# Kernel optimization log

Measured on AMD Instinct MI355X. Metric: run time of the kernel, lower is better.

The kernel has to match this reference:

```python
import jax, jax.numpy as jnp
import numpy as np

DIM = 768
INNER = int(DIM * 0.125)  # 96
N_TOK = 8
EPS = 1e-5


def setup_inputs() -> dict:
    key = jax.random.key(0)
    ks = jax.random.split(key, 5)
    x = jax.random.normal(ks[0], (64, DIM, 32, 32), dtype=jnp.float32)
    gamma = jnp.ones((DIM,), jnp.float32)
    beta = jnp.zeros((DIM,), jnp.float32)
    w1 = jax.random.normal(ks[1], (DIM, INNER), jnp.float32) * 0.02
    b1 = jnp.zeros((INNER,), jnp.float32)
    w2 = jax.random.normal(ks[2], (INNER, N_TOK), jnp.float32) * 0.02
    b2 = jnp.zeros((N_TOK,), jnp.float32)
    return {"x": x, "gamma": gamma, "beta": beta, "w1": w1, "b1": b1, "w2": w2, "b2": b2}


def reference(x, gamma, beta, w1, b1, w2, b2):
    B, C, H, W = x.shape
    # torch: x.transpose(1, 3).reshape(B, H*W, C)  ([B,C,H,W] -> [B,W,H,C] -> [B,HW,C])
    t = jnp.transpose(x, (0, 3, 2, 1)).reshape(B, H * W, C)
    # LayerNorm over channel dim
    mu = jnp.mean(t, axis=-1, keepdims=True)
    var = jnp.mean(jnp.square(t - mu), axis=-1, keepdims=True)
    xn = (t - mu) * jax.lax.rsqrt(var + EPS) * gamma + beta  # [B, HW, C]
    # small MLP producing per-token attention logits
    h = jax.nn.gelu(xn @ w1 + b1, approximate=False)  # [B, HW, INNER]
    attn = jax.nn.softmax(h @ w2 + b2, axis=1)        # softmax across HW -> [B, HW, N]
    # (x.unsqueeze(-1) * attn).mean(dim=1) == einsum / HW, no [B,HW,C,N] intermediate
    out = jnp.einsum('bhc,bhn->bcn', xn, attn) / (H * W)  # [B, C, N]
    return out
```

## Files before the change

kernel.cpp:

```cpp
#include <hip/hip_runtime.h>
#include <math.h>

#define BATCH 64
#define CH    768
#define NP    1024
#define NI    96
#define NT    8
#define EPSF  1e-5f

typedef __attribute__((ext_vector_type(8))) short  short8;
typedef __attribute__((ext_vector_type(4))) float  f32x4;

__device__ __forceinline__ unsigned short f2bf(float f) {
    unsigned int u = __float_as_uint(f);
    u += 0x7FFFu + ((u >> 16) & 1u);
    return (unsigned short)(u >> 16);
}

__global__ __launch_bounds__(64) void k_w1pack(const float* __restrict__ w1,
                                               unsigned short* __restrict__ w1f) {
    int ks = blockIdx.x / 6, nt = blockIdx.x % 6;
    int l  = threadIdx.x;
    int n  = nt * 16 + (l & 15);
    int k0 = ks * 32 + (l >> 4) * 8;
    unsigned short o[8];
#pragma unroll
    for (int j = 0; j < 8; ++j) o[j] = f2bf(w1[(size_t)(k0 + j) * NI + n]);
    unsigned short* dst = w1f + ((size_t)blockIdx.x * 64 + l) * 8;
#pragma unroll
    for (int j = 0; j < 8; ++j) dst[j] = o[j];
}

__global__ __launch_bounds__(256) void k_stats(const float* __restrict__ x,
                                               float2* __restrict__ stats) {
    int bid = blockIdx.x;
    int b   = bid >> 4;
    int p0  = (bid & 15) << 6;
    int lt  = threadIdx.x & 15;
    int cg  = threadIdx.x >> 4;
    const float* xb = x + (size_t)b * CH * NP + p0 + lt * 4;
    float4 s = make_float4(0.f,0.f,0.f,0.f);
    float4 q = make_float4(0.f,0.f,0.f,0.f);
#pragma unroll 4
    for (int c = cg; c < CH; c += 16) {
        float4 v = *(const float4*)(xb + (size_t)c * NP);
        s.x += v.x; s.y += v.y; s.z += v.z; s.w += v.w;
        q.x += v.x*v.x; q.y += v.y*v.y; q.z += v.z*v.z; q.w += v.w*v.w;
    }
    __shared__ float4 ls[16][16];
    __shared__ float4 lq[16][16];
    ls[cg][lt] = s; lq[cg][lt] = q;
    __syncthreads();
    for (int st = 8; st > 0; st >>= 1) {
        if (cg < st) {
            float4 s2 = ls[cg + st][lt], q2 = lq[cg + st][lt];
            s.x += s2.x; s.y += s2.y; s.z += s2.z; s.w += s2.w;
            q.x += q2.x; q.y += q2.y; q.z += q2.z; q.w += q2.w;
            ls[cg][lt] = s; lq[cg][lt] = q;
        }
        __syncthreads();
    }
    if (cg == 0) {
        const float inv = 1.0f / (float)CH;
        float2* st = stats + (size_t)b * NP + p0 + lt * 4;
        float mu, var;
        mu = s.x * inv; var = q.x * inv - mu * mu; st[0] = make_float2(mu, rsqrtf(var + EPSF));
        mu = s.y * inv; var = q.y * inv - mu * mu; st[1] = make_float2(mu, rsqrtf(var + EPSF));
        mu = s.z * inv; var = q.z * inv - mu * mu; st[2] = make_float2(mu, rsqrtf(var + EPSF));
        mu = s.w * inv; var = q.w * inv - mu * mu; st[3] = make_float2(mu, rsqrtf(var + EPSF));
    }
}

__global__ __launch_bounds__(256) void k_mlp(const float* __restrict__ x,
        const float2* __restrict__ stats,
        const float* __restrict__ gamma, const float* __restrict__ beta,
        const unsigned short* __restrict__ w1f,
        const float* __restrict__ b1, const float* __restrict__ w2,
        const float* __restrict__ b2, float* __restrict__ logits)
{
    int bid  = blockIdx.x;
    int b    = bid >> 3;
    int p0   = (bid & 7) << 7;
    int wv   = threadIdx.x >> 6;
    int lane = threadIdx.x & 63;
    int m    = lane & 15;
    int kg   = lane >> 4;
    int mt   = p0 + wv * 32;

    float2 st0 = stats[(size_t)b * NP + mt + m];
    float2 st1 = stats[(size_t)b * NP + mt + 16 + m];
    const float* xb = x + (size_t)b * CH * NP + mt + m;

    f32x4 accA[6], accB[6];
#pragma unroll
    for (int nt = 0; nt < 6; ++nt) {
        accA[nt] = (f32x4){0.f,0.f,0.f,0.f};
        accB[nt] = (f32x4){0.f,0.f,0.f,0.f};
    }
    const short8* wfp = (const short8*)w1f;

    for (int ks = 0; ks < 24; ++ks) {
        int cb = ks * 32 + kg * 8;
        const float* xc = xb + (size_t)cb * NP;
        float xv0[8], xv1[8];
#pragma unroll
        for (int j = 0; j < 8; ++j) {
            xv0[j] = xc[(size_t)j * NP];
            xv1[j] = xc[(size_t)j * NP + 16];
        }
        float4 g0 = *(const float4*)(gamma + cb);
        float4 g1 = *(const float4*)(gamma + cb + 4);
        float4 e0 = *(const float4*)(beta  + cb);
        float4 e1 = *(const float4*)(beta  + cb + 4);
        float gm[8] = {g0.x,g0.y,g0.z,g0.w,g1.x,g1.y,g1.z,g1.w};
        float bt[8] = {e0.x,e0.y,e0.z,e0.w,e1.x,e1.y,e1.z,e1.w};
        short8 a0, a1;
#pragma unroll
        for (int j = 0; j < 8; ++j) {
            float r0 = st0.y * gm[j];
            float r1 = st1.y * gm[j];
            float x0 = fmaf(xv0[j], r0, bt[j] - st0.x * r0);
            float x1 = fmaf(xv1[j], r1, bt[j] - st1.x * r1);
            a0[j] = (short)f2bf(x0);
            a1[j] = (short)f2bf(x1);
        }
        const short8* wk = wfp + (size_t)ks * 6 * 64 + lane;
#pragma unroll
        for (int nt = 0; nt < 6; ++nt) {
            short8 bf = wk[nt * 64];
            accA[nt] = __builtin_amdgcn_mfma_f32_16x16x32_bf16(a0, bf, accA[nt], 0, 0, 0);
            accB[nt] = __builtin_amdgcn_mfma_f32_16x16x32_bf16(a1, bf, accB[nt], 0, 0, 0);
        }
    }

    int nlo = lane & 15;
    float4 b2a = *(const float4*)b2;
    float4 b2b = *(const float4*)(b2 + 4);
#pragma unroll
    for (int half = 0; half < 2; ++half) {
        float lg[4][8];
#pragma unroll
        for (int r = 0; r < 4; ++r)
#pragma unroll
            for (int t = 0; t < 8; ++t) lg[r][t] = 0.f;
#pragma unroll
        for (int nt = 0; nt < 6; ++nt) {
            int n = nt * 16 + nlo;
            float b1v = b1[n];
            float4 w2a = *(const float4*)(w2 + n * 8);
            float4 w2b = *(const float4*)(w2 + n * 8 + 4);
            f32x4 ac = half ? accB[nt] : accA[nt];
#pragma unroll
            for (int r = 0; r < 4; ++r) {
                float h = ac[r] + b1v;
                h = 0.5f * h * (1.0f + erff(h * 0.70710678118654752f));
                lg[r][0] += h * w2a.x; lg[r][1] += h * w2a.y;
                lg[r][2] += h * w2a.z; lg[r][3] += h * w2a.w;
                lg[r][4] += h * w2b.x; lg[r][5] += h * w2b.y;
                lg[r][6] += h * w2b.z; lg[r][7] += h * w2b.w;
            }
        }
#pragma unroll
        for (int mask = 1; mask <= 8; mask <<= 1)
#pragma unroll
            for (int r = 0; r < 4; ++r)
#pragma unroll
                for (int t = 0; t < 8; ++t)
                    lg[r][t] += __shfl_xor(lg[r][t], mask, 64);
        if (nlo == 0) {
#pragma unroll
            for (int r = 0; r < 4; ++r) {
                int pp = mt + half * 16 + kg * 4 + r;
                float* op = logits + ((size_t)b * NP + pp) * NT;
                *(float4*)op       = make_float4(lg[r][0] + b2a.x, lg[r][1] + b2a.y,
                                                 lg[r][2] + b2a.z, lg[r][3] + b2a.w);
                *(float4*)(op + 4) = make_float4(lg[r][4] + b2b.x, lg[r][5] + b2b.y,
                                                 lg[r][6] + b2b.z, lg[r][7] + b2b.w);
            }
        }
    }
}

__global__ __launch_bounds__(256) void k_out(const float* __restrict__ x,
        const float* __restrict__ logits, const float2* __restrict__ stats,
        const float* __restrict__ gamma, const float* __restrict__ beta,
        float* __restrict__ out)
{
    int b   = blockIdx.x / 12;
    int c0  = (blockIdx.x % 12) * 64;
    int tid = threadIdx.x;
    int lane = tid & 63, wv = tid >> 6;
    __shared__ float gT[NT][NP];
    __shared__ float red[4][16];

    const float* lgp = logits + (size_t)b * NP * NT;
    const float2* stb = stats + (size_t)b * NP;
    float e[4][NT];
    float2 st4[4];
#pragma unroll
    for (int k = 0; k < 4; ++k) {
        int p = tid + 256 * k;
        float4 a  = *(const float4*)(lgp + (size_t)p * NT);
        float4 bq = *(const float4*)(lgp + (size_t)p * NT + 4);
        e[k][0]=a.x; e[k][1]=a.y; e[k][2]=a.z; e[k][3]=a.w;
        e[k][4]=bq.x; e[k][5]=bq.y; e[k][6]=bq.z; e[k][7]=bq.w;
        st4[k] = stb[p];
    }
    float mx[NT];
#pragma unroll
    for (int t = 0; t < NT; ++t)
        mx[t] = fmaxf(fmaxf(e[0][t], e[1][t]), fmaxf(e[2][t], e[3][t]));
#pragma unroll
    for (int mask = 1; mask <= 32; mask <<= 1)
#pragma unroll
        for (int t = 0; t < NT; ++t)
            mx[t] = fmaxf(mx[t], __shfl_xor(mx[t], mask, 64));
    if (lane == 0) {
#pragma unroll
        for (int t = 0; t < NT; ++t) red[wv][t] = mx[t];
    }
    __syncthreads();
#pragma unroll
    for (int t = 0; t < NT; ++t)
        mx[t] = fmaxf(fmaxf(red[0][t], red[1][t]), fmaxf(red[2][t], red[3][t]));
    __syncthreads();

    float sm[NT], s2p[NT];
#pragma unroll
    for (int t = 0; t < NT; ++t) { sm[t] = 0.f; s2p[t] = 0.f; }
#pragma unroll
    for (int k = 0; k < 4; ++k) {
        float mr = st4[k].x * st4[k].y;
#pragma unroll
        for (int t = 0; t < NT; ++t) {
            e[k][t] = expf(e[k][t] - mx[t]);
            sm[t]  += e[k][t];
            s2p[t] += mr * e[k][t];
        }
    }
#pragma unroll
    for (int mask = 1; mask <= 32; mask <<= 1)
#pragma unroll
        for (int t = 0; t < NT; ++t) {
            sm[t]  += __shfl_xor(sm[t],  mask, 64);
            s2p[t] += __shfl_xor(s2p[t], mask, 64);
        }
    if (lane == 0) {
#pragma unroll
        for (int t = 0; t < NT; ++t) { red[wv][t] = sm[t]; red[wv][8 + t] = s2p[t]; }
    }
    __syncthreads();
    float inv[NT], s2f[NT];
#pragma unroll
    for (int t = 0; t < NT; ++t) {
        float s  = red[0][t] + red[1][t] + red[2][t] + red[3][t];
        float s2 = red[0][8+t] + red[1][8+t] + red[2][8+t] + red[3][8+t];
        inv[t] = 1.0f / s;
        s2f[t] = s2 * inv[t];
    }
#pragma unroll
    for (int k = 0; k < 4; ++k)
#pragma unroll
        for (int t = 0; t < NT; ++t)
            gT[t][tid + 256 * k] = st4[k].y * e[k][t] * inv[t];
    __syncthreads();

    float greg[16][NT];
#pragma unroll
    for (int k2 = 0; k2 < 16; ++k2)
#pragma unroll
        for (int t = 0; t < NT; ++t)
            greg[k2][t] = gT[t][lane + 64 * k2];

    const float sc = 1.0f / (float)NP;
    for (int ch = 0; ch < 16; ++ch) {
        int c = c0 + wv * 16 + ch;
        const float* xr = x + ((size_t)b * CH + c) * NP;
        float xvv[16];
#pragma unroll
        for (int k2 = 0; k2 < 16; ++k2) xvv[k2] = xr[k2 * 64 + lane];
        float a[NT];
#pragma unroll
        for (int t = 0; t < NT; ++t) a[t] = 0.f;
#pragma unroll
        for (int k2 = 0; k2 < 16; ++k2)
#pragma unroll
            for (int t = 0; t < NT; ++t)
                a[t] = fmaf(xvv[k2], greg[k2][t], a[t]);
#pragma unroll
        for (int mask = 1; mask <= 32; mask <<= 1)
#pragma unroll
            for (int t = 0; t < NT; ++t)
                a[t] += __shfl_xor(a[t], mask, 64);
        if (lane == 0) {
            float ga = gamma[c] * sc, be = beta[c] * sc;
            float* op = out + ((size_t)b * CH + c) * NT;
            *(float4*)op       = make_float4(ga*(a[0]-s2f[0])+be, ga*(a[1]-s2f[1])+be,
                                             ga*(a[2]-s2f[2])+be, ga*(a[3]-s2f[3])+be);
            *(float4*)(op + 4) = make_float4(ga*(a[4]-s2f[4])+be, ga*(a[5]-s2f[5])+be,
                                             ga*(a[6]-s2f[6])+be, ga*(a[7]-s2f[7])+be);
        }
    }
}

extern "C" void kernel_launch(void* const* d_in, const int* in_sizes, int n_in,
                              void* d_out, int out_size, void* d_ws, size_t ws_size,
                              hipStream_t stream) {
    const float* x     = (const float*)d_in[0];
    const float* gamma = (const float*)d_in[1];
    const float* beta  = (const float*)d_in[2];
    const float* w1    = (const float*)d_in[3];
    const float* b1    = (const float*)d_in[4];
    const float* w2    = (const float*)d_in[5];
    const float* b2    = (const float*)d_in[6];
    float* out = (float*)d_out;

    char* ws = (char*)d_ws;
    float2*         stats  = (float2*)ws;
    float*          lgbuf  = (float*)(ws + (size_t)BATCH*NP*sizeof(float2));
    unsigned short* w1f    = (unsigned short*)(ws + (size_t)BATCH*NP*sizeof(float2)
                                                  + (size_t)BATCH*NP*NT*sizeof(float));

    k_w1pack<<<24 * 6,     64,  0, stream>>>(w1, w1f);
    k_stats <<<BATCH * 16, 256, 0, stream>>>(x, stats);
    k_mlp   <<<BATCH * 8,  256, 0, stream>>>(x, stats, gamma, beta, w1f, b1, w2, b2, lgbuf);
    k_out   <<<BATCH * 12, 256, 0, stream>>>(x, lgbuf, stats, gamma, beta, out);
}
```

Before: 381.0 us.

## Fuse LayerNorm stats into MLP kernel and compute output via bf16 MFMA

Folds the per-token mean/rstd computation into the MLP kernel, so each block computes stats for its 128 tokens and keeps them in shared memory. This removes the separate stats launch, though x is still read twice inside the block. The output einsum is split into a small per-batch kernel, which builds the softmax-weighted matrix and packs it into bf16 MFMA B-fragments, and an output kernel that runs the x·g contraction on bf16 matrix cores instead of scalar FMAs with shuffle reductions. This trades fp32 accuracy in the final reduction for matrix-core throughput and adds one extra launch with only 64 blocks.

```diff
diff --git a/kernel.cpp b/kernel.cpp
--- a/kernel.cpp
+++ b/kernel.cpp
@@ -1,4 +1,5 @@
 #include <hip/hip_runtime.h>
+#include <hip/hip_bf16.h>
 #include <math.h>
 
 #define BATCH 64
@@ -11,10 +12,9 @@
 typedef __attribute__((ext_vector_type(8))) short  short8;
 typedef __attribute__((ext_vector_type(4))) float  f32x4;
 
-__device__ __forceinline__ unsigned short f2bf(float f) {
-    unsigned int u = __float_as_uint(f);
-    u += 0x7FFFu + ((u >> 16) & 1u);
-    return (unsigned short)(u >> 16);
+__device__ __forceinline__ short bfs(float f) {
+    __hip_bfloat16 h = __float2bfloat16(f);
+    return *reinterpret_cast<short*>(&h);
 }
 
 __global__ __launch_bounds__(64) void k_w1pack(const float* __restrict__ w1,
@@ -23,72 +23,71 @@
     int l  = threadIdx.x;
     int n  = nt * 16 + (l & 15);
     int k0 = ks * 32 + (l >> 4) * 8;
-    unsigned short o[8];
-#pragma unroll
-    for (int j = 0; j < 8; ++j) o[j] = f2bf(w1[(size_t)(k0 + j) * NI + n]);
-    unsigned short* dst = w1f + ((size_t)blockIdx.x * 64 + l) * 8;
-#pragma unroll
-    for (int j = 0; j < 8; ++j) dst[j] = o[j];
-}
-
-__global__ __launch_bounds__(256) void k_stats(const float* __restrict__ x,
-                                               float2* __restrict__ stats) {
-    int bid = blockIdx.x;
-    int b   = bid >> 4;
-    int p0  = (bid & 15) << 6;
-    int lt  = threadIdx.x & 15;
-    int cg  = threadIdx.x >> 4;
-    const float* xb = x + (size_t)b * CH * NP + p0 + lt * 4;
-    float4 s = make_float4(0.f,0.f,0.f,0.f);
-    float4 q = make_float4(0.f,0.f,0.f,0.f);
-#pragma unroll 4
-    for (int c = cg; c < CH; c += 16) {
-        float4 v = *(const float4*)(xb + (size_t)c * NP);
-        s.x += v.x; s.y += v.y; s.z += v.z; s.w += v.w;
-        q.x += v.x*v.x; q.y += v.y*v.y; q.z += v.z*v.z; q.w += v.w*v.w;
-    }
-    __shared__ float4 ls[16][16];
-    __shared__ float4 lq[16][16];
-    ls[cg][lt] = s; lq[cg][lt] = q;
-    __syncthreads();
-    for (int st = 8; st > 0; st >>= 1) {
-        if (cg < st) {
-            float4 s2 = ls[cg + st][lt], q2 = lq[cg + st][lt];
-            s.x += s2.x; s.y += s2.y; s.z += s2.z; s.w += s2.w;
-            q.x += q2.x; q.y += q2.y; q.z += q2.z; q.w += q2.w;
-            ls[cg][lt] = s; lq[cg][lt] = q;
-        }
-        __syncthreads();
-    }
-    if (cg == 0) {
-        const float inv = 1.0f / (float)CH;
-        float2* st = stats + (size_t)b * NP + p0 + lt * 4;
-        float mu, var;
-        mu = s.x * inv; var = q.x * inv - mu * mu; st[0] = make_float2(mu, rsqrtf(var + EPSF));
-        mu = s.y * inv; var = q.y * inv - mu * mu; st[1] = make_float2(mu, rsqrtf(var + EPSF));
-        mu = s.z * inv; var = q.z * inv - mu * mu; st[2] = make_float2(mu, rsqrtf(var + EPSF));
-        mu = s.w * inv; var = q.w * inv - mu * mu; st[3] = make_float2(mu, rsqrtf(var + EPSF));
-    }
-}
-
-__global__ __launch_bounds__(256) void k_mlp(const float* __restrict__ x,
-        const float2* __restrict__ stats,
+    short8 o;
+#pragma unroll
+    for (int j = 0; j < 8; ++j) o[j] = bfs(w1[(size_t)(k0 + j) * NI + n]);
+    *(short8*)(w1f + ((size_t)blockIdx.x * 64 + l) * 8) = o;
+}
+
+__global__ __launch_bounds__(256) void k_mlpf(const float* __restrict__ x,
         const float* __restrict__ gamma, const float* __restrict__ beta,
         const unsigned short* __restrict__ w1f,
         const float* __restrict__ b1, const float* __restrict__ w2,
-        const float* __restrict__ b2, float* __restrict__ logits)
+        const float* __restrict__ b2,
+        float2* __restrict__ stats, float* __restrict__ logits)
 {
-    int bid  = blockIdx.x;
-    int b    = bid >> 3;
-    int p0   = (bid & 7) << 7;
-    int wv   = threadIdx.x >> 6;
-    int lane = threadIdx.x & 63;
+    int bid = blockIdx.x;
+    int b   = bid >> 3;
+    int p0  = (bid & 7) << 7;
+    int tid = threadIdx.x;
+
+    __shared__ float4 ls[8][32];
+    __shared__ float4 lq[8][32];
+    __shared__ float2 stl[128];
+
+    {
+        int tg = tid & 31;
+        int cg = tid >> 5;
+        const float* xb = x + (size_t)b * CH * NP + p0 + tg * 4;
+        float4 s = make_float4(0.f,0.f,0.f,0.f);
+        float4 q = make_float4(0.f,0.f,0.f,0.f);
+#pragma unroll 4
+        for (int c = cg; c < CH; c += 8) {
+            float4 v = *(const float4*)(xb + (size_t)c * NP);
+            s.x += v.x; s.y += v.y; s.z += v.z; s.w += v.w;
+            q.x += v.x*v.x; q.y += v.y*v.y; q.z += v.z*v.z; q.w += v.w*v.w;
+        }
+        ls[cg][tg] = s; lq[cg][tg] = q;
+        __syncthreads();
+        if (cg == 0) {
+#pragma unroll
+            for (int k = 1; k < 8; ++k) {
+                float4 s2 = ls[k][tg], q2 = lq[k][tg];
+                s.x += s2.x; s.y += s2.y; s.z += s2.z; s.w += s2.w;
+                q.x += q2.x; q.y += q2.y; q.z += q2.z; q.w += q2.w;
+            }
+            const float inv = 1.0f / (float)CH;
+            float2 r0, r1, r2, r3;
+            float mu, var;
+            mu = s.x*inv; var = q.x*inv - mu*mu; r0 = make_float2(mu, rsqrtf(var + EPSF));
+            mu = s.y*inv; var = q.y*inv - mu*mu; r1 = make_float2(mu, rsqrtf(var + EPSF));
+            mu = s.z*inv; var = q.z*inv - mu*mu; r2 = make_float2(mu, rsqrtf(var + EPSF));
+            mu = s.w*inv; var = q.w*inv - mu*mu; r3 = make_float2(mu, rsqrtf(var + EPSF));
+            stl[tg*4+0] = r0; stl[tg*4+1] = r1; stl[tg*4+2] = r2; stl[tg*4+3] = r3;
+            float2* st = stats + (size_t)b * NP + p0 + tg * 4;
+            st[0] = r0; st[1] = r1; st[2] = r2; st[3] = r3;
+        }
+        __syncthreads();
+    }
+
+    int wv   = tid >> 6;
+    int lane = tid & 63;
     int m    = lane & 15;
     int kg   = lane >> 4;
     int mt   = p0 + wv * 32;
 
-    float2 st0 = stats[(size_t)b * NP + mt + m];
-    float2 st1 = stats[(size_t)b * NP + mt + 16 + m];
+    float2 st0 = stl[wv * 32 + m];
+    float2 st1 = stl[wv * 32 + 16 + m];
     const float* xb = x + (size_t)b * CH * NP + mt + m;
 
     f32x4 accA[6], accB[6];
@@ -117,12 +116,10 @@
         short8 a0, a1;
 #pragma unroll
         for (int j = 0; j < 8; ++j) {
-            float r0 = st0.y * gm[j];
-            float r1 = st1.y * gm[j];
-            float x0 = fmaf(xv0[j], r0, bt[j] - st0.x * r0);
-            float x1 = fmaf(xv1[j], r1, bt[j] - st1.x * r1);
-            a0[j] = (short)f2bf(x0);
-            a1[j] = (short)f2bf(x1);
+            float rg0 = st0.y * gm[j];
+            float rg1 = st1.y * gm[j];
+            a0[j] = bfs(fmaf(xv0[j], rg0, fmaf(-st0.x, rg0, bt[j])));
+            a1[j] = bfs(fmaf(xv1[j], rg1, fmaf(-st1.x, rg1, bt[j])));
         }
         const short8* wk = wfp + (size_t)ks * 6 * 64 + lane;
 #pragma unroll
@@ -181,16 +178,14 @@
     }
 }
 
-__global__ __launch_bounds__(256) void k_out(const float* __restrict__ x,
-        const float* __restrict__ logits, const float2* __restrict__ stats,
-        const float* __restrict__ gamma, const float* __restrict__ beta,
-        float* __restrict__ out)
+__global__ __launch_bounds__(256) void k_g(const float* __restrict__ logits,
+        const float2* __restrict__ stats,
+        unsigned short* __restrict__ gbf, float* __restrict__ S2)
 {
-    int b   = blockIdx.x / 12;
-    int c0  = (blockIdx.x % 12) * 64;
+    int b = blockIdx.x;
     int tid = threadIdx.x;
     int lane = tid & 63, wv = tid >> 6;
-    __shared__ float gT[NT][NP];
+    __shared__ float gs[NP][NT];
     __shared__ float red[4][16];
 
     const float* lgp = logits + (size_t)b * NP * NT;
@@ -258,47 +253,73 @@
         inv[t] = 1.0f / s;
         s2f[t] = s2 * inv[t];
     }
+    if (tid < NT) S2[b * NT + tid] = s2f[tid];
+
 #pragma unroll
     for (int k = 0; k < 4; ++k)
 #pragma unroll
         for (int t = 0; t < NT; ++t)
-            gT[t][tid + 256 * k] = st4[k].y * e[k][t] * inv[t];
+            gs[tid + 256 * k][t] = st4[k].y * e[k][t] * inv[t];
     __syncthreads();
 
-    float greg[16][NT];
-#pragma unroll
-    for (int k2 = 0; k2 < 16; ++k2)
-#pragma unroll
-        for (int t = 0; t < NT; ++t)
-            greg[k2][t] = gT[t][lane + 64 * k2];
-
-    const float sc = 1.0f / (float)NP;
-    for (int ch = 0; ch < 16; ++ch) {
-        int c = c0 + wv * 16 + ch;
-        const float* xr = x + ((size_t)b * CH + c) * NP;
-        float xvv[16];
-#pragma unroll
-        for (int k2 = 0; k2 < 16; ++k2) xvv[k2] = xr[k2 * 64 + lane];
-        float a[NT];
-#pragma unroll
-        for (int t = 0; t < NT; ++t) a[t] = 0.f;
-#pragma unroll
-        for (int k2 = 0; k2 < 16; ++k2)
-#pragma unroll
-            for (int t = 0; t < NT; ++t)
-                a[t] = fmaf(xvv[k2], greg[k2][t], a[t]);
-#pragma unroll
-        for (int mask = 1; mask <= 32; mask <<= 1)
-#pragma unroll
-            for (int t = 0; t < NT; ++t)
-                a[t] += __shfl_xor(a[t], mask, 64);
-        if (lane == 0) {
-            float ga = gamma[c] * sc, be = beta[c] * sc;
-            float* op = out + ((size_t)b * CH + c) * NT;
-            *(float4*)op       = make_float4(ga*(a[0]-s2f[0])+be, ga*(a[1]-s2f[1])+be,
-                                             ga*(a[2]-s2f[2])+be, ga*(a[3]-s2f[3])+be);
-            *(float4*)(op + 4) = make_float4(ga*(a[4]-s2f[4])+be, ga*(a[5]-s2f[5])+be,
-                                             ga*(a[6]-s2f[6])+be, ga*(a[7]-s2f[7])+be);
+    unsigned short* gb = gbf + (size_t)b * 2048 * 8;
+#pragma unroll
+    for (int ss = 0; ss < 8; ++ss) {
+        int slot   = tid * 8 + ss;
+        int lane_s = slot & 63;
+        int ks     = slot >> 6;
+        int n      = lane_s & 15;
+        int k0     = ks * 32 + (lane_s >> 4) * 8;
+        short8 o = (short8){0,0,0,0,0,0,0,0};
+        if (n < 8) {
+#pragma unroll
+            for (int j = 0; j < 8; ++j) o[j] = bfs(gs[k0 + j][n]);
+        }
+        *(short8*)(gb + (size_t)slot * 8) = o;
+    }
+}
+
+__global__ __launch_bounds__(256) void k_outg(const float* __restrict__ x,
+        const unsigned short* __restrict__ gbf, const float* __restrict__ S2,
+        const float* __restrict__ gamma, const float* __restrict__ beta,
+        float* __restrict__ out)
+{
+    int b   = blockIdx.x / 12;
+    int c0  = (blockIdx.x % 12) * 64;
+    int tid = threadIdx.x, lane = tid & 63, wv = tid >> 6;
+    int kg  = lane >> 4, m = lane & 15, n = lane & 15;
+    int cw  = c0 + wv * 16;
+
+    const float*  xr = x + ((size_t)b * CH + cw + m) * NP + kg * 8;
+    const short8* gb = (const short8*)gbf + (size_t)b * 2048;
+
+    f32x4 acc0 = (f32x4){0.f,0.f,0.f,0.f};
+    f32x4 acc1 = (f32x4){0.f,0.f,0.f,0.f};
+#pragma unroll 4
+    for (int ks = 0; ks < 32; ks += 2) {
+        float4 v0 = *(const float4*)(xr + ks * 32);
+        float4 v1 = *(const float4*)(xr + ks * 32 + 4);
+        float4 v2 = *(const float4*)(xr + ks * 32 + 32);
+        float4 v3 = *(const float4*)(xr + ks * 32 + 36);
+        short8 a0, a1;
+        a0[0]=bfs(v0.x); a0[1]=bfs(v0.y); a0[2]=bfs(v0.z); a0[3]=bfs(v0.w);
+        a0[4]=bfs(v1.x); a0[5]=bfs(v1.y); a0[6]=bfs(v1.z); a0[7]=bfs(v1.w);
+        a1[0]=bfs(v2.x); a1[1]=bfs(v2.y); a1[2]=bfs(v2.z); a1[3]=bfs(v2.w);
+        a1[4]=bfs(v3.x); a1[5]=bfs(v3.y); a1[6]=bfs(v3.z); a1[7]=bfs(v3.w);
+        short8 bf0 = gb[ks * 64 + lane];
+        short8 bf1 = gb[(ks + 1) * 64 + lane];
+        acc0 = __builtin_amdgcn_mfma_f32_16x16x32_bf16(a0, bf0, acc0, 0, 0, 0);
+        acc1 = __builtin_amdgcn_mfma_f32_16x16x32_bf16(a1, bf1, acc1, 0, 0, 0);
+    }
+
+    if (n < NT) {
+        float s2v = S2[b * NT + n];
+        const float sc = 1.0f / (float)NP;
+#pragma unroll
+        for (int r = 0; r < 4; ++r) {
+            int c = cw + kg * 4 + r;
+            float val = acc0[r] + acc1[r];
+            out[((size_t)b * CH + c) * NT + n] = (gamma[c] * (val - s2v) + beta[c]) * sc;
         }
     }
 }
@@ -316,13 +337,14 @@
     float* out = (float*)d_out;
 
     char* ws = (char*)d_ws;
-    float2*         stats  = (float2*)ws;
-    float*          lgbuf  = (float*)(ws + (size_t)BATCH*NP*sizeof(float2));
-    unsigned short* w1f    = (unsigned short*)(ws + (size_t)BATCH*NP*sizeof(float2)
-                                                  + (size_t)BATCH*NP*NT*sizeof(float));
+    float2*         stats = (float2*)(ws + 0);
+    float*          lgbuf = (float*)(ws + 524288);
+    unsigned short* w1f   = (unsigned short*)(ws + 2621440);
+    unsigned short* gbf   = (unsigned short*)(ws + 2768896);
+    float*          S2    = (float*)(ws + 4866048);
 
     k_w1pack<<<24 * 6,     64,  0, stream>>>(w1, w1f);
-    k_stats <<<BATCH * 16, 256, 0, stream>>>(x, stats);
-    k_mlp   <<<BATCH * 8,  256, 0, stream>>>(x, stats, gamma, beta, w1f, b1, w2, b2, lgbuf);
-    k_out   <<<BATCH * 12, 256, 0, stream>>>(x, lgbuf, stats, gamma, beta, out);
-}
+    k_mlpf  <<<BATCH * 8,  256, 0, stream>>>(x, gamma, beta, w1f, b1, w2, b2, stats, lgbuf);
+    k_g     <<<BATCH,      256, 0, stream>>>(lgbuf, stats, gbf, S2);
+    k_outg  <<<BATCH * 12, 256, 0, stream>>>(x, gbf, S2, gamma, beta, out);
+}
```

New measurement: 353.8 us. 7.1% less time.
